# Kernel optimization log

Measured on AMD Instinct MI355X. Metric: run time of the kernel, lower is better.

Reference implementation:

```python
import jax, jax.numpy as jnp
from jax import lax
import numpy as np

B, CIN, HC, K, REC = 64, 64, 64, 3, 5
MG = 240 // REC  # 48
EPS = 1e-8


def conv2d(x, w, b, pad):
    y = lax.conv_general_dilated(x, w, (1, 1), [(pad, pad), (pad, pad)],
                                 dimension_numbers=('NCHW', 'OIHW', 'NCHW'))
    return y + b[None, :, None, None]


def conv_transpose2d(x, w, b, stride, pad):
    # PyTorch ConvTranspose2d: w is (Cin, Cout, kH, kW)
    k = w.shape[2]
    w_t = jnp.transpose(w[:, :, ::-1, ::-1], (1, 0, 2, 3))  # -> OIHW, flipped
    y = lax.conv_general_dilated(x, w_t, (1, 1),
                                 [(k - 1 - pad, k - 1 - pad)] * 2,
                                 lhs_dilation=(stride, stride),
                                 dimension_numbers=('NCHW', 'OIHW', 'NCHW'))
    return y + b[None, :, None, None]


def leaky(x):
    return jnp.where(x >= 0, x, 0.2 * x)


def setup_inputs() -> dict:
    key = jax.random.key(0)
    ks = jax.random.split(key, 12)
    s = 0.05
    return {
        'x': jax.random.normal(ks[0], (B, CIN, 64, 64), jnp.float32),
        'h': jax.random.normal(ks[1], (B, HC, 64, 64), jnp.float32),
        'c': jax.random.normal(ks[2], (B, HC, 64, 64), jnp.float32),
        'recalled_memory_feature': jax.random.normal(ks[3], (B, REC, MG, 32, 32), jnp.float32),
        'conv_w': jax.random.normal(ks[4], (5 * HC, CIN + HC, K, K), jnp.float32) * s,
        'conv_b': jax.random.normal(ks[5], (5 * HC,), jnp.float32) * s,
        'convc_w': jax.random.normal(ks[6], (MG, HC, 1, 1), jnp.float32) * s,
        'convc_b': jax.random.normal(ks[7], (MG,), jnp.float32) * s,
        'convssm_w': jax.random.normal(ks[8], (MG, MG, 4, 4), jnp.float32) * s,
        'convssm_b': jax.random.normal(ks[9], (MG,), jnp.float32) * s,
        'convfuse_w': jax.random.normal(ks[10], (HC, MG + HC, 1, 1), jnp.float32) * s,
        'convfuse_b': jax.random.normal(ks[11], (HC,), jnp.float32) * s,
    }


def reference(x, h, c, recalled_memory_feature, conv_w, conv_b, convc_w, convc_b,
              convssm_w, convssm_b, convfuse_w, convfuse_b):
    rm = recalled_memory_feature.reshape(B, REC, MG, 32, 32)
    rm_avg = rm.mean(axis=(3, 4))                      # (B, REC, MG)
    q = leaky(conv2d(c, convc_w, convc_b, 0))          # (B, MG, 64, 64)
    q_avg = q.mean(axis=(2, 3))                        # (B, MG)
    # cosine similarity along channel dim, vectorized over (B, REC)
    qn = jnp.maximum(jnp.linalg.norm(q_avg, axis=1, keepdims=True), EPS)   # (B,1)
    mn = jnp.maximum(jnp.linalg.norm(rm_avg, axis=2), EPS)                  # (B,REC)
    cos = jnp.einsum('bm,brm->br', q_avg, rm_avg) / (qn * mn)               # (B,REC)
    attn = jax.nn.softmax(cos, axis=1)                                      # (B,REC)
    mt = jnp.einsum('br,brmhw->bmhw', attn, rm)        # (B, MG, 32, 32)
    mt = leaky(conv_transpose2d(mt, convssm_w, convssm_b, 2, 1))  # (B, MG, 64, 64)

    gates = conv2d(jnp.concatenate((x, h), axis=1), conv_w, conv_b, K // 2)
    i, f, g, o, lam = jnp.split(gates, 5, axis=1)
    i = jax.nn.sigmoid(i)
    f = jax.nn.sigmoid(f)
    o = jax.nn.sigmoid(o)
    g = jnp.tanh(g)
    lam = jax.nn.sigmoid(lam)
    c_new = f * c + i * g
    h_new = o * jnp.tanh(conv2d(jnp.concatenate((c_new, mt), axis=1), convfuse_w, convfuse_b, 0))
    h_out = lam * h_new + (1.0 - lam) * h
    return (h_out, c_new)
```

## Files before the change

kernel.cpp:

```cpp
#include <hip/hip_runtime.h>
#include <hip/hip_bf16.h>
#include <cstdint>

#define HW 4096
#define MGc 48
#define RECc 5

typedef __attribute__((ext_vector_type(8))) short bf16x8;
typedef __attribute__((ext_vector_type(4))) float f32x4;

__device__ __forceinline__ float sigf(float x) { return 1.f / (1.f + expf(-x)); }
__device__ __forceinline__ float leakyf(float x) { return x >= 0.f ? x : 0.2f * x; }
__device__ __forceinline__ unsigned short f2bfu(float f) {
  __hip_bfloat16 b = __float2bfloat16(f);
  return *reinterpret_cast<unsigned short*>(&b);
}
__device__ __forceinline__ float bfu2f(unsigned short u) {
  unsigned v = ((unsigned)u) << 16;
  return __uint_as_float(v);
}
__device__ __forceinline__ void gload_lds16(const void* g, void* l) {
  __builtin_amdgcn_global_load_lds(
      (const __attribute__((address_space(1))) unsigned int*)g,
      (__attribute__((address_space(3))) unsigned int*)l, 16, 0, 0);
}

__global__ __launch_bounds__(256) void k_att(const float* __restrict__ rm,
    float* __restrict__ rm_sum, const float* __restrict__ c,
    const float* __restrict__ ccw, const float* __restrict__ ccb,
    float* __restrict__ q_part) {
  __shared__ __align__(16) char smem[13568];
  int bid = blockIdx.x, tid = threadIdx.x;
  if (bid < 15360) {
    float* sred = (float*)smem;
    int row = bid;
    const float4* p = reinterpret_cast<const float4*>(rm + (size_t)row * 1024);
    float4 v = p[tid];
    float s = v.x + v.y + v.z + v.w;
    #pragma unroll
    for (int off = 32; off; off >>= 1) s += __shfl_down(s, off);
    if ((tid & 63) == 0) sred[tid >> 6] = s;
    __syncthreads();
    if (tid == 0) rm_sum[row] = sred[0] + sred[1] + sred[2] + sred[3];
  } else {
    float* wl = (float*)smem;
    float* bl = wl + MGc * 64;
    float (*red)[MGc] = (float(*)[MGc])(bl + 64);
    int r = bid - 15360;
    int seg = r & 15, b = r >> 4;
    for (int i = tid; i < MGc * 64; i += 256) wl[i] = ccw[i];
    if (tid < MGc) bl[tid] = ccb[tid];
    __syncthreads();
    int px = seg * 256 + tid;
    float acc[MGc];
    #pragma unroll
    for (int m = 0; m < MGc; m++) acc[m] = 0.f;
    const float* cp = c + (size_t)b * 64 * HW + px;
    for (int ci = 0; ci < 64; ci++) {
      float v = cp[(size_t)ci * HW];
      #pragma unroll
      for (int m = 0; m < MGc; m++) acc[m] += wl[m * 64 + ci] * v;
    }
    int lane = tid & 63, wv = tid >> 6;
    #pragma unroll
    for (int m = 0; m < MGc; m++) {
      float t2 = leakyf(acc[m] + bl[m]);
      #pragma unroll
      for (int off = 32; off; off >>= 1) t2 += __shfl_down(t2, off);
      if (lane == 0) red[wv][m] = t2;
    }
    __syncthreads();
    if (tid < MGc) {
      float t2 = red[0][tid] + red[1][tid] + red[2][tid] + red[3][tid];
      q_part[((size_t)b * 16 + seg) * MGc + tid] = t2;
    }
  }
}

__global__ __launch_bounds__(256) void k_mid(const float* __restrict__ rm,
    const float* __restrict__ rm_sum, const float* __restrict__ q_part,
    float* __restrict__ mt_pre, const float* __restrict__ cw,
    __hip_bfloat16* __restrict__ Wp, __hip_bfloat16* __restrict__ Pp,
    const float* __restrict__ xin, const float* __restrict__ hin) {
  __shared__ __align__(16) char smem[16704];
  int bid = blockIdx.x, tid = threadIdx.x;
  if (bid < 12288) {
    float* sat = (float*)smem;
    int idx = bid * 256 + tid;
    int b = idx / (MGc * 1024);
    if (tid < 64) {
      int lane = tid;
      float q = 0.f;
      if (lane < MGc) {
        float s = 0.f;
        for (int sg = 0; sg < 16; sg++) s += q_part[((size_t)b * 16 + sg) * MGc + lane];
        q = s * (1.f / 4096.f);
      }
      float qs = q * q;
      #pragma unroll
      for (int off = 32; off; off >>= 1) qs += __shfl_xor(qs, off);
      float qn = fmaxf(sqrtf(qs), 1e-8f);
      float cosv[RECc];
      #pragma unroll
      for (int r = 0; r < RECc; r++) {
        float m = 0.f;
        if (lane < MGc) m = rm_sum[((size_t)b * RECc + r) * MGc + lane] * (1.f / 1024.f);
        float d = q * m, ms = m * m;
        #pragma unroll
        for (int off = 32; off; off >>= 1) { d += __shfl_xor(d, off); ms += __shfl_xor(ms, off); }
        float mn = fmaxf(sqrtf(ms), 1e-8f);
        cosv[r] = d / (qn * mn);
      }
      float mx = cosv[0];
      #pragma unroll
      for (int r = 1; r < RECc; r++) mx = fmaxf(mx, cosv[r]);
      float ssum = 0.f;
      #pragma unroll
      for (int r = 0; r < RECc; r++) { cosv[r] = expf(cosv[r] - mx); ssum += cosv[r]; }
      float inv = 1.f / ssum;
      #pragma unroll
      for (int r = 0; r < RECc; r++)
        if (lane == r) sat[r] = cosv[r] * inv;
    }
    __syncthreads();
    int rem = idx - b * (MGc * 1024);
    const float* base = rm + (size_t)b * RECc * MGc * 1024 + rem;
    float v = sat[0] * base[0] + sat[1] * base[MGc * 1024] + sat[2] * base[2 * MGc * 1024]
            + sat[3] * base[3 * MGc * 1024] + sat[4] * base[4 * MGc * 1024];
    mt_pre[idx] = v;
  } else if (bid < 13728) {
    int idx = (bid - 12288) * 256 + tid;
    int t = idx / (320 * 128);
    int rem = idx % (320 * 128);
    int ocp = rem / 128, ci = rem % 128;
    int nt = ocp / 80, r2 = ocp % 80, gate = r2 / 16, ml = r2 % 16;
    int oc = gate * 64 + nt * 16 + ml;
    Wp[idx] = __float2bfloat16(cw[((size_t)oc * 128 + ci) * 9 + t]);
  } else if (bid < 14768) {
    int idx = (bid - 13728) * 256 + tid;
    int b = idx / 4160, i = idx % 4160;
    bf16x8* base = reinterpret_cast<bf16x8*>(Pp);
    size_t u;
    if (i < 2112) {
      int r = (i < 1056) ? 0 : 65;
      int j = (i < 1056) ? i : i - 1056;
      u = ((size_t)b * 66 + r) * 1056 + j;
    } else {
      int i2 = i - 2112;
      int row = 1 + (i2 >> 5), k = i2 & 31;
      int px = (k < 16) ? 0 : 65, ci8 = k & 15;
      u = (((size_t)b * 66 + row) * 66 + px) * 16 + ci8;
    }
    base[u] = (bf16x8)0;
  } else {
    float (*t)[65] = (float(*)[65])smem;
    int r = bid - 14768;
    int half = r & 1, y = (r >> 1) & 63, b = r >> 7;
    const float* src = (half ? hin : xin) + (size_t)b * 64 * HW + y * 64;
    #pragma unroll
    for (int it = 0; it < 4; it++) {
      int li = it * 256 + tid;
      int ci = li >> 4, x4 = (li & 15) * 4;
      float4 v = *reinterpret_cast<const float4*>(src + (size_t)ci * HW + x4);
      t[x4][ci] = v.x; t[x4 + 1][ci] = v.y; t[x4 + 2][ci] = v.z; t[x4 + 3][ci] = v.w;
    }
    __syncthreads();
    int x = tid >> 2, c16 = (tid & 3) * 16;
    unsigned short* dst = reinterpret_cast<unsigned short*>(Pp) +
        ((((size_t)b * 66 + y + 1) * 66 + x + 1) * 128 + half * 64 + c16);
    bf16x8 o0, o1;
    #pragma unroll
    for (int j = 0; j < 8; j++) {
      o0[j] = (short)f2bfu(t[x][c16 + j]);
      o1[j] = (short)f2bfu(t[x][c16 + 8 + j]);
    }
    *reinterpret_cast<bf16x8*>(dst) = o0;
    *reinterpret_cast<bf16x8*>(dst + 8) = o1;
  }
}

__global__ __launch_bounds__(512) void k_ssm(const float* __restrict__ mt_pre,
    const float* __restrict__ w, const float* __restrict__ bias,
    __hip_bfloat16* __restrict__ mt) {
  __shared__ float in_t[12][10][20];
  __shared__ float w_t[12][48][16];
  int b = blockIdx.y;
  int tile = blockIdx.x;
  int y0 = (tile >> 1) * 16, x0 = (tile & 1) * 32;
  int wv = threadIdx.x >> 6, lane = threadIdx.x & 63;
  int co0 = wv * 6;
  int oyl = lane >> 2, xseg = lane & 3;
  int oy = y0 + oyl;
  int iy0 = (y0 >> 1) - 1, ix0 = (x0 >> 1) - 1;
  int kyA = (oy + 1) & 1;
  int iyA = (oy + 1 - kyA) >> 1;
  int rA = iyA - iy0, rB = rA - 1;
  float acc[6][8] = {};
  for (int ch = 0; ch < 4; ch++) {
    int ci0 = ch * 12;
    __syncthreads();
    for (int i = threadIdx.x; i < 12 * 10 * 18; i += 512) {
      int ci = i / 180, rr = (i % 180) / 18, cc2 = i % 18;
      int giy = iy0 + rr, gix = ix0 + cc2;
      float v = 0.f;
      if ((unsigned)giy < 32u && (unsigned)gix < 32u)
        v = mt_pre[(((size_t)b * MGc + ci0 + ci) * 32 + giy) * 32 + gix];
      in_t[ci][rr][cc2] = v;
    }
    for (int i = threadIdx.x; i < 12 * 48 * 16; i += 512)
      (&w_t[0][0][0])[i] = w[ci0 * 768 + i];
    __syncthreads();
    #pragma unroll 1
    for (int ci = 0; ci < 12; ci++) {
      float4 a0 = *reinterpret_cast<const float4*>(&in_t[ci][rA][xseg * 4]);
      float4 a1 = *reinterpret_cast<const float4*>(&in_t[ci][rA][xseg * 4 + 4]);
      float4 b0 = *reinterpret_cast<const float4*>(&in_t[ci][rB][xseg * 4]);
      float4 b1 = *reinterpret_cast<const float4*>(&in_t[ci][rB][xseg * 4 + 4]);
      float vA[6] = {a0.x, a0.y, a0.z, a0.w, a1.x, a1.y};
      float vB[6] = {b0.x, b0.y, b0.z, b0.w, b1.x, b1.y};
      #pragma unroll
      for (int co = 0; co < 6; co++) {
        const float* wp = &w_t[ci][co0 + co][0];
        float4 wA = *reinterpret_cast<const float4*>(wp + kyA * 4);
        float4 wB = *reinterpret_cast<const float4*>(wp + (kyA + 2) * 4);
        #pragma unroll
        for (int j = 0; j < 8; j++) {
          if ((j & 1) == 0) {
            int hi = (j >> 1) + 1, lo = j >> 1;
            acc[co][j] += vA[hi] * wA.y + vA[lo] * wA.w + vB[hi] * wB.y + vB[lo] * wB.w;
          } else {
            int hi = ((j + 1) >> 1) + 1, lo = (j + 1) >> 1;
            acc[co][j] += vA[hi] * wA.x + vA[lo] * wA.z + vB[hi] * wB.x + vB[lo] * wB.z;
          }
        }
      }
    }
  }
  int oxb = x0 + xseg * 8;
  #pragma unroll
  for (int co = 0; co < 6; co++) {
    float bb = bias[co0 + co];
    size_t obase = (((size_t)b * MGc + co0 + co) * 64 + oy) * 64 + oxb;
    #pragma unroll
    for (int j = 0; j < 8; j++)
      mt[obase + j] = __float2bfloat16(leakyf(acc[co][j] + bb));
  }
}

__global__ __launch_bounds__(256) void k_gates_mfma(
    const __hip_bfloat16* __restrict__ Pp, const __hip_bfloat16* __restrict__ Wp,
    const float* __restrict__ c, const float* __restrict__ cb,
    float* __restrict__ c_new, __hip_bfloat16* __restrict__ o_g,
    __hip_bfloat16* __restrict__ lam_g) {
  __shared__ bf16x8 s_in[1296];
  __shared__ bf16x8 s_w[2880];
  int orig = blockIdx.y * gridDim.x + blockIdx.x;
  int t_id = (orig & 7) * 512 + (orig >> 3);
  int b = t_id >> 6;
  int r6 = t_id & 63;
  int ytile = r6 >> 4, xtile = (r6 >> 2) & 3, nt = r6 & 3;
  int y0 = ytile * 16, x0 = xtile * 16;
  int tid = threadIdx.x;
  int wv = tid >> 6, lane = tid & 63;
  int lane15 = lane & 15, lq = lane >> 4;

  const char* Pb = (const char*)Pp;
  const char* Wb = (const char*)Wp;

  const char* gin[6]; int din[6]; bool ain[6];
  #pragma unroll
  for (int k = 0; k < 6; k++) {
    int u = wv + 4 * k;
    int e = u * 64 + lane;
    ain[k] = (u < 21) && (e < 1296);
    int ee = (e < 1296) ? e : 0;
    int L = ee / 72, r = ee - L * 72;
    int llq = r / 18, xi = r - llq * 18;
    gin[k] = Pb + ((((size_t)b * 66 + y0 + L) * 66 + (x0 + xi)) * 256) + llq * 16;
    din[k] = ee;
  }
  const char* gw[12]; int dw[12]; bool aw[12];
  #pragma unroll
  for (int k = 0; k < 12; k++) {
    int u = wv + 4 * k;
    aw[k] = (u < 45);
    int uu = (u < 45) ? u : 0;
    int e = uu * 64 + lane;
    int unit = e / 80, ol = e - unit * 80;
    int t = unit >> 2, g = unit & 3;
    gw[k] = Wb + (((size_t)t * 320 + nt * 80 + ol) * 128 + g * 8) * 2;
    dw[k] = e;
  }

  f32x4 acc[4][5];
  #pragma unroll
  for (int i = 0; i < 4; i++)
    #pragma unroll
    for (int j = 0; j < 5; j++) acc[i][j] = (f32x4)0.f;

  #pragma unroll 1
  for (int cc = 0; cc < 4; cc++) {
    __syncthreads();
    int co = cc * 64;
    #pragma unroll
    for (int k = 0; k < 6; k++)
      if (ain[k]) gload_lds16(gin[k] + co, (void*)&s_in[din[k]]);
    #pragma unroll
    for (int k = 0; k < 12; k++)
      if (aw[k]) gload_lds16(gw[k] + co, (void*)&s_w[dw[k]]);
    __syncthreads();

    #pragma unroll
    for (int dx = 0; dx < 3; dx++) {
      bf16x8 af[6];
      #pragma unroll
      for (int r = 0; r < 6; r++)
        af[r] = s_in[((wv * 4 + r) * 4 + lq) * 18 + lane15 + dx];
      #pragma unroll
      for (int ky = 0; ky < 3; ky++) {
        int t = ky * 3 + dx;
        bf16x8 bw[5];
        #pragma unroll
        for (int gg = 0; gg < 5; gg++)
          bw[gg] = s_w[(t * 4 + lq) * 80 + gg * 16 + lane15];
        __builtin_amdgcn_s_setprio(1);
        #pragma unroll
        for (int rr = 0; rr < 4; rr++)
          #pragma unroll
          for (int gg = 0; gg < 5; gg++)
            acc[rr][gg] = __builtin_amdgcn_mfma_f32_16x16x32_bf16(
                af[rr + ky], bw[gg], acc[rr][gg], 0, 0, 0);
        __builtin_amdgcn_s_setprio(0);
      }
    }
  }

  int m_hid = nt * 16 + lane15;
  float bi = cb[m_hid], bff = cb[64 + m_hid], bgg = cb[128 + m_hid],
        bo = cb[192 + m_hid], bl = cb[256 + m_hid];
  int xb = x0 + lq * 4;
  size_t chofs = ((size_t)b * 64 + m_hid) * HW;
  #pragma unroll
  for (int rr = 0; rr < 4; rr++) {
    int y = y0 + wv * 4 + rr;
    size_t pofs = chofs + (size_t)y * 64 + xb;
    f32x4 cold = *reinterpret_cast<const f32x4*>(c + pofs);
    f32x4 cn;
    unsigned short ov[4], lv[4];
    #pragma unroll
    for (int e = 0; e < 4; e++) {
      float i_ = sigf(acc[rr][0][e] + bi);
      float f_ = sigf(acc[rr][1][e] + bff);
      float g_ = tanhf(acc[rr][2][e] + bgg);
      float o_ = sigf(acc[rr][3][e] + bo);
      float l_ = sigf(acc[rr][4][e] + bl);
      cn[e] = f_ * cold[e] + i_ * g_;
      ov[e] = f2bfu(o_);
      lv[e] = f2bfu(l_);
    }
    *reinterpret_cast<f32x4*>(c_new + pofs) = cn;
    ushort4 ovv = {ov[0], ov[1], ov[2], ov[3]};
    ushort4 lvv = {lv[0], lv[1], lv[2], lv[3]};
    *reinterpret_cast<ushort4*>(reinterpret_cast<unsigned short*>(o_g) + pofs) = ovv;
    *reinterpret_cast<ushort4*>(reinterpret_cast<unsigned short*>(lam_g) + pofs) = lvv;
  }
}

__global__ __launch_bounds__(256) void k_fuse(const float* __restrict__ c_new,
    const __hip_bfloat16* __restrict__ mt, const __hip_bfloat16* __restrict__ o_g,
    const __hip_bfloat16* __restrict__ lam_g, const float* __restrict__ h,
    const float* __restrict__ fw, const float* __restrict__ fb,
    float* __restrict__ h_out) {
  __shared__ float wl[112][32];
  int b = blockIdx.y;
  int seg = blockIdx.x & 7, chalf = blockIdx.x >> 3;
  int co0 = chalf * 32;
  for (int i = threadIdx.x; i < 112 * 32; i += 256) {
    int ci = i >> 5, co = i & 31;
    wl[ci][co] = fw[(co0 + co) * 112 + ci];
  }
  __syncthreads();
  int px = seg * 512 + threadIdx.x * 2;
  size_t bofs = (size_t)b * 64 * HW;
  float2 acc[32];
  #pragma unroll
  for (int co = 0; co < 32; co++) { float bv = fb[co0 + co]; acc[co].x = bv; acc[co].y = bv; }
  #pragma unroll 1
  for (int ci = 0; ci < 64; ci++) {
    float2 v = *reinterpret_cast<const float2*>(c_new + bofs + (size_t)ci * HW + px);
    #pragma unroll
    for (int c4 = 0; c4 < 8; c4++) {
      float4 w = *reinterpret_cast<const float4*>(&wl[ci][c4 * 4]);
      acc[c4 * 4 + 0].x += w.x * v.x; acc[c4 * 4 + 0].y += w.x * v.y;
      acc[c4 * 4 + 1].x += w.y * v.x; acc[c4 * 4 + 1].y += w.y * v.y;
      acc[c4 * 4 + 2].x += w.z * v.x; acc[c4 * 4 + 2].y += w.z * v.y;
      acc[c4 * 4 + 3].x += w.w * v.x; acc[c4 * 4 + 3].y += w.w * v.y;
    }
  }
  const unsigned short* mtu = reinterpret_cast<const unsigned short*>(mt);
  size_t mtofs = (size_t)b * MGc * HW + px;
  #pragma unroll 1
  for (int ci = 0; ci < 48; ci++) {
    unsigned u = *reinterpret_cast<const unsigned*>(mtu + mtofs + (size_t)ci * HW);
    float vx = bfu2f((unsigned short)(u & 0xffff));
    float vy = bfu2f((unsigned short)(u >> 16));
    #pragma unroll
    for (int c4 = 0; c4 < 8; c4++) {
      float4 w = *reinterpret_cast<const float4*>(&wl[64 + ci][c4 * 4]);
      acc[c4 * 4 + 0].x += w.x * vx; acc[c4 * 4 + 0].y += w.x * vy;
      acc[c4 * 4 + 1].x += w.y * vx; acc[c4 * 4 + 1].y += w.y * vy;
      acc[c4 * 4 + 2].x += w.z * vx; acc[c4 * 4 + 2].y += w.z * vy;
      acc[c4 * 4 + 3].x += w.w * vx; acc[c4 * 4 + 3].y += w.w * vy;
    }
  }
  const unsigned short* ou = reinterpret_cast<const unsigned short*>(o_g);
  const unsigned short* lu = reinterpret_cast<const unsigned short*>(lam_g);
  #pragma unroll
  for (int co = 0; co < 32; co++) {
    size_t ofs = bofs + (size_t)(co0 + co) * HW + px;
    unsigned uo = *reinterpret_cast<const unsigned*>(ou + ofs);
    unsigned ul = *reinterpret_cast<const unsigned*>(lu + ofs);
    float2 hv = *reinterpret_cast<const float2*>(h + ofs);
    float hnx = tanhf(acc[co].x), hny = tanhf(acc[co].y);
    float ox = bfu2f((unsigned short)(uo & 0xffff)), oy = bfu2f((unsigned short)(uo >> 16));
    float lx = bfu2f((unsigned short)(ul & 0xffff)), ly = bfu2f((unsigned short)(ul >> 16));
    float2 r;
    r.x = lx * (ox * hnx) + (1.f - lx) * hv.x;
    r.y = ly * (oy * hny) + (1.f - ly) * hv.y;
    *reinterpret_cast<float2*>(h_out + ofs) = r;
  }
}

extern "C" void kernel_launch(void* const* d_in, const int* in_sizes, int n_in,
                              void* d_out, int out_size, void* d_ws, size_t ws_size,
                              hipStream_t stream) {
  const float* x   = (const float*)d_in[0];
  const float* h   = (const float*)d_in[1];
  const float* c   = (const float*)d_in[2];
  const float* rm  = (const float*)d_in[3];
  const float* cw  = (const float*)d_in[4];
  const float* cb  = (const float*)d_in[5];
  const float* ccw = (const float*)d_in[6];
  const float* ccb = (const float*)d_in[7];
  const float* sw  = (const float*)d_in[8];
  const float* sb  = (const float*)d_in[9];
  const float* fw  = (const float*)d_in[10];
  const float* fb  = (const float*)d_in[11];

  float* h_out = (float*)d_out;
  float* c_new = h_out + (size_t)16777216;

  char* ws = (char*)d_ws;
  float* rm_sum = (float*)(ws + 0);
  float* q_part = (float*)(ws + 65536);
  __hip_bfloat16* o_g   = (__hip_bfloat16*)(ws + 0);
  __hip_bfloat16* lam_g = (__hip_bfloat16*)(ws + 33554432);
  __hip_bfloat16* mt    = (__hip_bfloat16*)(ws + 67108864);
  __hip_bfloat16* Pp    = (__hip_bfloat16*)(ws + 92274688);
  __hip_bfloat16* Wp    = (__hip_bfloat16*)(ws + 163643392);
  float* mt_pre = h_out;

  k_att<<<16384, 256, 0, stream>>>(rm, rm_sum, c, ccw, ccb, q_part);
  k_mid<<<22960, 256, 0, stream>>>(rm, rm_sum, q_part, mt_pre, cw, Wp, Pp, x, h);
  k_ssm<<<dim3(8, 64), 512, 0, stream>>>(mt_pre, sw, sb, mt);
  k_gates_mfma<<<dim3(64, 64), 256, 0, stream>>>(Pp, Wp, c, cb, c_new, o_g, lam_g);
  k_fuse<<<dim3(16, 64), 256, 0, stream>>>(c_new, mt, o_g, lam_g, h, fw, fb, h_out);
}
```

Measured before the change: 637.4 us.

## Merge SSM transposed-conv into gates MFMA launch and widen fuse per-thread work

```diff
diff --git a/kernel.cpp b/kernel.cpp
--- a/kernel.cpp
+++ b/kernel.cpp
@@ -23,6 +23,9 @@
   __builtin_amdgcn_global_load_lds(
       (const __attribute__((address_space(1))) unsigned int*)g,
       (__attribute__((address_space(3))) unsigned int*)l, 16, 0, 0);
+}
+__device__ __forceinline__ void fma4(f32x4& a, float w, const f32x4& v) {
+  a[0] += w * v[0]; a[1] += w * v[1]; a[2] += w * v[2]; a[3] += w * v[3];
 }
 
 __global__ __launch_bounds__(256) void k_att(const float* __restrict__ rm,
@@ -179,190 +182,190 @@
   }
 }
 
-__global__ __launch_bounds__(512) void k_ssm(const float* __restrict__ mt_pre,
-    const float* __restrict__ w, const float* __restrict__ bias,
-    __hip_bfloat16* __restrict__ mt) {
-  __shared__ float in_t[12][10][20];
-  __shared__ float w_t[12][48][16];
-  int b = blockIdx.y;
-  int tile = blockIdx.x;
-  int y0 = (tile >> 1) * 16, x0 = (tile & 1) * 32;
-  int wv = threadIdx.x >> 6, lane = threadIdx.x & 63;
-  int co0 = wv * 6;
-  int oyl = lane >> 2, xseg = lane & 3;
-  int oy = y0 + oyl;
-  int iy0 = (y0 >> 1) - 1, ix0 = (x0 >> 1) - 1;
-  int kyA = (oy + 1) & 1;
-  int iyA = (oy + 1 - kyA) >> 1;
-  int rA = iyA - iy0, rB = rA - 1;
-  float acc[6][8] = {};
-  for (int ch = 0; ch < 4; ch++) {
-    int ci0 = ch * 12;
-    __syncthreads();
-    for (int i = threadIdx.x; i < 12 * 10 * 18; i += 512) {
-      int ci = i / 180, rr = (i % 180) / 18, cc2 = i % 18;
-      int giy = iy0 + rr, gix = ix0 + cc2;
-      float v = 0.f;
-      if ((unsigned)giy < 32u && (unsigned)gix < 32u)
-        v = mt_pre[(((size_t)b * MGc + ci0 + ci) * 32 + giy) * 32 + gix];
-      in_t[ci][rr][cc2] = v;
-    }
-    for (int i = threadIdx.x; i < 12 * 48 * 16; i += 512)
-      (&w_t[0][0][0])[i] = w[ci0 * 768 + i];
-    __syncthreads();
-    #pragma unroll 1
-    for (int ci = 0; ci < 12; ci++) {
-      float4 a0 = *reinterpret_cast<const float4*>(&in_t[ci][rA][xseg * 4]);
-      float4 a1 = *reinterpret_cast<const float4*>(&in_t[ci][rA][xseg * 4 + 4]);
-      float4 b0 = *reinterpret_cast<const float4*>(&in_t[ci][rB][xseg * 4]);
-      float4 b1 = *reinterpret_cast<const float4*>(&in_t[ci][rB][xseg * 4 + 4]);
-      float vA[6] = {a0.x, a0.y, a0.z, a0.w, a1.x, a1.y};
-      float vB[6] = {b0.x, b0.y, b0.z, b0.w, b1.x, b1.y};
-      #pragma unroll
-      for (int co = 0; co < 6; co++) {
-        const float* wp = &w_t[ci][co0 + co][0];
-        float4 wA = *reinterpret_cast<const float4*>(wp + kyA * 4);
-        float4 wB = *reinterpret_cast<const float4*>(wp + (kyA + 2) * 4);
-        #pragma unroll
-        for (int j = 0; j < 8; j++) {
-          if ((j & 1) == 0) {
-            int hi = (j >> 1) + 1, lo = j >> 1;
-            acc[co][j] += vA[hi] * wA.y + vA[lo] * wA.w + vB[hi] * wB.y + vB[lo] * wB.w;
-          } else {
-            int hi = ((j + 1) >> 1) + 1, lo = (j + 1) >> 1;
-            acc[co][j] += vA[hi] * wA.x + vA[lo] * wA.z + vB[hi] * wB.x + vB[lo] * wB.z;
-          }
-        }
-      }
-    }
-  }
-  int oxb = x0 + xseg * 8;
-  #pragma unroll
-  for (int co = 0; co < 6; co++) {
-    float bb = bias[co0 + co];
-    size_t obase = (((size_t)b * MGc + co0 + co) * 64 + oy) * 64 + oxb;
-    #pragma unroll
-    for (int j = 0; j < 8; j++)
-      mt[obase + j] = __float2bfloat16(leakyf(acc[co][j] + bb));
-  }
-}
-
-__global__ __launch_bounds__(256) void k_gates_mfma(
+__global__ __launch_bounds__(256) void k_main(
     const __hip_bfloat16* __restrict__ Pp, const __hip_bfloat16* __restrict__ Wp,
     const float* __restrict__ c, const float* __restrict__ cb,
     float* __restrict__ c_new, __hip_bfloat16* __restrict__ o_g,
-    __hip_bfloat16* __restrict__ lam_g) {
-  __shared__ bf16x8 s_in[1296];
-  __shared__ bf16x8 s_w[2880];
-  int orig = blockIdx.y * gridDim.x + blockIdx.x;
-  int t_id = (orig & 7) * 512 + (orig >> 3);
-  int b = t_id >> 6;
-  int r6 = t_id & 63;
-  int ytile = r6 >> 4, xtile = (r6 >> 2) & 3, nt = r6 & 3;
-  int y0 = ytile * 16, x0 = xtile * 16;
-  int tid = threadIdx.x;
-  int wv = tid >> 6, lane = tid & 63;
-  int lane15 = lane & 15, lq = lane >> 4;
-
-  const char* Pb = (const char*)Pp;
-  const char* Wb = (const char*)Wp;
-
-  const char* gin[6]; int din[6]; bool ain[6];
-  #pragma unroll
-  for (int k = 0; k < 6; k++) {
-    int u = wv + 4 * k;
-    int e = u * 64 + lane;
-    ain[k] = (u < 21) && (e < 1296);
-    int ee = (e < 1296) ? e : 0;
-    int L = ee / 72, r = ee - L * 72;
-    int llq = r / 18, xi = r - llq * 18;
-    gin[k] = Pb + ((((size_t)b * 66 + y0 + L) * 66 + (x0 + xi)) * 256) + llq * 16;
-    din[k] = ee;
-  }
-  const char* gw[12]; int dw[12]; bool aw[12];
-  #pragma unroll
-  for (int k = 0; k < 12; k++) {
-    int u = wv + 4 * k;
-    aw[k] = (u < 45);
-    int uu = (u < 45) ? u : 0;
-    int e = uu * 64 + lane;
-    int unit = e / 80, ol = e - unit * 80;
-    int t = unit >> 2, g = unit & 3;
-    gw[k] = Wb + (((size_t)t * 320 + nt * 80 + ol) * 128 + g * 8) * 2;
-    dw[k] = e;
-  }
-
-  f32x4 acc[4][5];
-  #pragma unroll
-  for (int i = 0; i < 4; i++)
-    #pragma unroll
-    for (int j = 0; j < 5; j++) acc[i][j] = (f32x4)0.f;
-
-  #pragma unroll 1
-  for (int cc = 0; cc < 4; cc++) {
-    __syncthreads();
-    int co = cc * 64;
-    #pragma unroll
-    for (int k = 0; k < 6; k++)
-      if (ain[k]) gload_lds16(gin[k] + co, (void*)&s_in[din[k]]);
-    #pragma unroll
-    for (int k = 0; k < 12; k++)
-      if (aw[k]) gload_lds16(gw[k] + co, (void*)&s_w[dw[k]]);
-    __syncthreads();
-
-    #pragma unroll
-    for (int dx = 0; dx < 3; dx++) {
-      bf16x8 af[6];
-      #pragma unroll
-      for (int r = 0; r < 6; r++)
-        af[r] = s_in[((wv * 4 + r) * 4 + lq) * 18 + lane15 + dx];
-      #pragma unroll
-      for (int ky = 0; ky < 3; ky++) {
-        int t = ky * 3 + dx;
-        bf16x8 bw[5];
+    __hip_bfloat16* __restrict__ lam_g,
+    const float* __restrict__ mt_pre, const float* __restrict__ sw,
+    const float* __restrict__ sb, __hip_bfloat16* __restrict__ mt) {
+  __shared__ __align__(16) char arena[66816];
+  int bid = blockIdx.x, tid = threadIdx.x;
+  if (bid < 4096) {
+    bf16x8* s_in = (bf16x8*)arena;
+    bf16x8* s_w  = (bf16x8*)(arena + 20736);
+    int t_id = (bid & 7) * 512 + (bid >> 3);
+    int b = t_id >> 6;
+    int r6 = t_id & 63;
+    int ytile = r6 >> 4, xtile = (r6 >> 2) & 3, nt = r6 & 3;
+    int y0 = ytile * 16, x0 = xtile * 16;
+    int wv = tid >> 6, lane = tid & 63;
+    int lane15 = lane & 15, lq = lane >> 4;
+
+    const char* Pb = (const char*)Pp;
+    const char* Wb = (const char*)Wp;
+
+    const char* gin[6]; int din[6]; bool ain[6];
+    #pragma unroll
+    for (int k = 0; k < 6; k++) {
+      int u = wv + 4 * k;
+      int e = u * 64 + lane;
+      ain[k] = (u < 21) && (e < 1296);
+      int ee = (e < 1296) ? e : 0;
+      int L = ee / 72, r = ee - L * 72;
+      int llq = r / 18, xi = r - llq * 18;
+      gin[k] = Pb + ((((size_t)b * 66 + y0 + L) * 66 + (x0 + xi)) * 256) + llq * 16;
+      din[k] = ee;
+    }
+    const char* gw[12]; int dw[12]; bool aw[12];
+    #pragma unroll
+    for (int k = 0; k < 12; k++) {
+      int u = wv + 4 * k;
+      aw[k] = (u < 45);
+      int uu = (u < 45) ? u : 0;
+      int e = uu * 64 + lane;
+      int unit = e / 80, ol = e - unit * 80;
+      int t = unit >> 2, g = unit & 3;
+      gw[k] = Wb + (((size_t)t * 320 + nt * 80 + ol) * 128 + g * 8) * 2;
+      dw[k] = e;
+    }
+
+    f32x4 acc[4][5];
+    #pragma unroll
+    for (int i = 0; i < 4; i++)
+      #pragma unroll
+      for (int j = 0; j < 5; j++) acc[i][j] = (f32x4)0.f;
+
+    #pragma unroll 1
+    for (int cc = 0; cc < 4; cc++) {
+      __syncthreads();
+      int co = cc * 64;
+      #pragma unroll
+      for (int k = 0; k < 6; k++)
+        if (ain[k]) gload_lds16(gin[k] + co, (void*)&s_in[din[k]]);
+      #pragma unroll
+      for (int k = 0; k < 12; k++)
+        if (aw[k]) gload_lds16(gw[k] + co, (void*)&s_w[dw[k]]);
+      __syncthreads();
+
+      #pragma unroll
+      for (int dx = 0; dx < 3; dx++) {
+        bf16x8 af[6];
         #pragma unroll
-        for (int gg = 0; gg < 5; gg++)
-          bw[gg] = s_w[(t * 4 + lq) * 80 + gg * 16 + lane15];
-        __builtin_amdgcn_s_setprio(1);
+        for (int r = 0; r < 6; r++)
+          af[r] = s_in[((wv * 4 + r) * 4 + lq) * 18 + lane15 + dx];
         #pragma unroll
-        for (int rr = 0; rr < 4; rr++)
+        for (int ky = 0; ky < 3; ky++) {
+          int t = ky * 3 + dx;
+          bf16x8 bw[5];
           #pragma unroll
           for (int gg = 0; gg < 5; gg++)
-            acc[rr][gg] = __builtin_amdgcn_mfma_f32_16x16x32_bf16(
-                af[rr + ky], bw[gg], acc[rr][gg], 0, 0, 0);
-        __builtin_amdgcn_s_setprio(0);
-      }
-    }
-  }
-
-  int m_hid = nt * 16 + lane15;
-  float bi = cb[m_hid], bff = cb[64 + m_hid], bgg = cb[128 + m_hid],
-        bo = cb[192 + m_hid], bl = cb[256 + m_hid];
-  int xb = x0 + lq * 4;
-  size_t chofs = ((size_t)b * 64 + m_hid) * HW;
-  #pragma unroll
-  for (int rr = 0; rr < 4; rr++) {
-    int y = y0 + wv * 4 + rr;
-    size_t pofs = chofs + (size_t)y * 64 + xb;
-    f32x4 cold = *reinterpret_cast<const f32x4*>(c + pofs);
-    f32x4 cn;
-    unsigned short ov[4], lv[4];
-    #pragma unroll
-    for (int e = 0; e < 4; e++) {
-      float i_ = sigf(acc[rr][0][e] + bi);
-      float f_ = sigf(acc[rr][1][e] + bff);
-      float g_ = tanhf(acc[rr][2][e] + bgg);
-      float o_ = sigf(acc[rr][3][e] + bo);
-      float l_ = sigf(acc[rr][4][e] + bl);
-      cn[e] = f_ * cold[e] + i_ * g_;
-      ov[e] = f2bfu(o_);
-      lv[e] = f2bfu(l_);
-    }
-    *reinterpret_cast<f32x4*>(c_new + pofs) = cn;
-    ushort4 ovv = {ov[0], ov[1], ov[2], ov[3]};
-    ushort4 lvv = {lv[0], lv[1], lv[2], lv[3]};
-    *reinterpret_cast<ushort4*>(reinterpret_cast<unsigned short*>(o_g) + pofs) = ovv;
-    *reinterpret_cast<ushort4*>(reinterpret_cast<unsigned short*>(lam_g) + pofs) = lvv;
+            bw[gg] = s_w[(t * 4 + lq) * 80 + gg * 16 + lane15];
+          __builtin_amdgcn_s_setprio(1);
+          #pragma unroll
+          for (int rr = 0; rr < 4; rr++)
+            #pragma unroll
+            for (int gg = 0; gg < 5; gg++)
+              acc[rr][gg] = __builtin_amdgcn_mfma_f32_16x16x32_bf16(
+                  af[rr + ky], bw[gg], acc[rr][gg], 0, 0, 0);
+          __builtin_amdgcn_s_setprio(0);
+        }
+      }
+    }
+
+    int m_hid = nt * 16 + lane15;
+    float bi = cb[m_hid], bff = cb[64 + m_hid], bgg = cb[128 + m_hid],
+          bo = cb[192 + m_hid], bl = cb[256 + m_hid];
+    int xb = x0 + lq * 4;
+    size_t chofs = ((size_t)b * 64 + m_hid) * HW;
+    #pragma unroll
+    for (int rr = 0; rr < 4; rr++) {
+      int y = y0 + wv * 4 + rr;
+      size_t pofs = chofs + (size_t)y * 64 + xb;
+      f32x4 cold = *reinterpret_cast<const f32x4*>(c + pofs);
+      f32x4 cn;
+      unsigned short ov[4], lv[4];
+      #pragma unroll
+      for (int e = 0; e < 4; e++) {
+        float i_ = sigf(acc[rr][0][e] + bi);
+        float f_ = sigf(acc[rr][1][e] + bff);
+        float g_ = tanhf(acc[rr][2][e] + bgg);
+        float o_ = sigf(acc[rr][3][e] + bo);
+        float l_ = sigf(acc[rr][4][e] + bl);
+        cn[e] = f_ * cold[e] + i_ * g_;
+        ov[e] = f2bfu(o_);
+        lv[e] = f2bfu(l_);
+      }
+      *reinterpret_cast<f32x4*>(c_new + pofs) = cn;
+      ushort4 ovv = {ov[0], ov[1], ov[2], ov[3]};
+      ushort4 lvv = {lv[0], lv[1], lv[2], lv[3]};
+      *reinterpret_cast<ushort4*>(reinterpret_cast<unsigned short*>(o_g) + pofs) = ovv;
+      *reinterpret_cast<ushort4*>(reinterpret_cast<unsigned short*>(lam_g) + pofs) = lvv;
+    }
+  } else {
+    float (*in_t)[10][20] = (float(*)[10][20])arena;
+    float (*w_t)[48][16]  = (float(*)[48][16])(arena + 9600);
+    int sbid = bid - 4096;
+    int tile = sbid & 7, b = sbid >> 3;
+    int y0 = (tile >> 1) * 16, x0 = (tile & 1) * 32;
+    int wv = tid >> 6, lane = tid & 63;
+    int co0 = wv * 12;
+    int oyl = lane >> 2, xseg = lane & 3;
+    int oy = y0 + oyl;
+    int iy0 = (y0 >> 1) - 1, ix0 = (x0 >> 1) - 1;
+    int kyA = (oy + 1) & 1;
+    int iyA = (oy + 1 - kyA) >> 1;
+    int rA = iyA - iy0, rB = rA - 1;
+    float acc[12][8] = {};
+    for (int ch = 0; ch < 4; ch++) {
+      int ci0 = ch * 12;
+      __syncthreads();
+      for (int i = tid; i < 12 * 10 * 18; i += 256) {
+        int ci = i / 180, rr = (i % 180) / 18, cc2 = i % 18;
+        int giy = iy0 + rr, gix = ix0 + cc2;
+        float v = 0.f;
+        if ((unsigned)giy < 32u && (unsigned)gix < 32u)
+          v = mt_pre[(((size_t)b * MGc + ci0 + ci) * 32 + giy) * 32 + gix];
+        in_t[ci][rr][cc2] = v;
+      }
+      for (int i = tid; i < 12 * 48 * 16; i += 256)
+        (&w_t[0][0][0])[i] = sw[ci0 * 768 + i];
+      __syncthreads();
+      #pragma unroll 1
+      for (int ci = 0; ci < 12; ci++) {
+        float4 a0 = *reinterpret_cast<const float4*>(&in_t[ci][rA][xseg * 4]);
+        float4 a1 = *reinterpret_cast<const float4*>(&in_t[ci][rA][xseg * 4 + 4]);
+        float4 b0 = *reinterpret_cast<const float4*>(&in_t[ci][rB][xseg * 4]);
+        float4 b1 = *reinterpret_cast<const float4*>(&in_t[ci][rB][xseg * 4 + 4]);
+        float vA[6] = {a0.x, a0.y, a0.z, a0.w, a1.x, a1.y};
+        float vB[6] = {b0.x, b0.y, b0.z, b0.w, b1.x, b1.y};
+        #pragma unroll
+        for (int co = 0; co < 12; co++) {
+          const float* wp = &w_t[ci][co0 + co][0];
+          float4 wA = *reinterpret_cast<const float4*>(wp + kyA * 4);
+          float4 wB = *reinterpret_cast<const float4*>(wp + (kyA + 2) * 4);
+          #pragma unroll
+          for (int j = 0; j < 8; j++) {
+            if ((j & 1) == 0) {
+              int hi = (j >> 1) + 1, lo = j >> 1;
+              acc[co][j] += vA[hi] * wA.y + vA[lo] * wA.w + vB[hi] * wB.y + vB[lo] * wB.w;
+            } else {
+              int hi = ((j + 1) >> 1) + 1, lo = (j + 1) >> 1;
+              acc[co][j] += vA[hi] * wA.x + vA[lo] * wA.z + vB[hi] * wB.x + vB[lo] * wB.z;
+            }
+          }
+        }
+      }
+    }
+    int oxb = x0 + xseg * 8;
+    #pragma unroll
+    for (int co = 0; co < 12; co++) {
+      float bb = sb[co0 + co];
+      size_t obase = (((size_t)b * MGc + co0 + co) * 64 + oy) * 64 + oxb;
+      #pragma unroll
+      for (int j = 0; j < 8; j++)
+        mt[obase + j] = __float2bfloat16(leakyf(acc[co][j] + bb));
+    }
   }
 }
 
@@ -373,44 +376,44 @@
     float* __restrict__ h_out) {
   __shared__ float wl[112][32];
   int b = blockIdx.y;
-  int seg = blockIdx.x & 7, chalf = blockIdx.x >> 3;
+  int seg = blockIdx.x & 3, chalf = blockIdx.x >> 2;
   int co0 = chalf * 32;
   for (int i = threadIdx.x; i < 112 * 32; i += 256) {
     int ci = i >> 5, co = i & 31;
     wl[ci][co] = fw[(co0 + co) * 112 + ci];
   }
   __syncthreads();
-  int px = seg * 512 + threadIdx.x * 2;
+  int px = seg * 1024 + threadIdx.x * 4;
   size_t bofs = (size_t)b * 64 * HW;
-  float2 acc[32];
+  f32x4 acc[32];
   #pragma unroll
-  for (int co = 0; co < 32; co++) { float bv = fb[co0 + co]; acc[co].x = bv; acc[co].y = bv; }
+  for (int co = 0; co < 32; co++) acc[co] = (f32x4)(fb[co0 + co]);
   #pragma unroll 1
   for (int ci = 0; ci < 64; ci++) {
-    float2 v = *reinterpret_cast<const float2*>(c_new + bofs + (size_t)ci * HW + px);
+    f32x4 v = *reinterpret_cast<const f32x4*>(c_new + bofs + (size_t)ci * HW + px);
     #pragma unroll
     for (int c4 = 0; c4 < 8; c4++) {
       float4 w = *reinterpret_cast<const float4*>(&wl[ci][c4 * 4]);
-      acc[c4 * 4 + 0].x += w.x * v.x; acc[c4 * 4 + 0].y += w.x * v.y;
-      acc[c4 * 4 + 1].x += w.y * v.x; acc[c4 * 4 + 1].y += w.y * v.y;
-      acc[c4 * 4 + 2].x += w.z * v.x; acc[c4 * 4 + 2].y += w.z * v.y;
-      acc[c4 * 4 + 3].x += w.w * v.x; acc[c4 * 4 + 3].y += w.w * v.y;
+      fma4(acc[c4 * 4 + 0], w.x, v);
+      fma4(acc[c4 * 4 + 1], w.y, v);
+      fma4(acc[c4 * 4 + 2], w.z, v);
+      fma4(acc[c4 * 4 + 3], w.w, v);
     }
   }
   const unsigned short* mtu = reinterpret_cast<const unsigned short*>(mt);
   size_t mtofs = (size_t)b * MGc * HW + px;
   #pragma unroll 1
   for (int ci = 0; ci < 48; ci++) {
-    unsigned u = *reinterpret_cast<const unsigned*>(mtu + mtofs + (size_t)ci * HW);
-    float vx = bfu2f((unsigned short)(u & 0xffff));
-    float vy = bfu2f((unsigned short)(u >> 16));
+    ushort4 u = *reinterpret_cast<const ushort4*>(mtu + mtofs + (size_t)ci * HW);
+    f32x4 v;
+    v[0] = bfu2f(u.x); v[1] = bfu2f(u.y); v[2] = bfu2f(u.z); v[3] = bfu2f(u.w);
     #pragma unroll
     for (int c4 = 0; c4 < 8; c4++) {
       float4 w = *reinterpret_cast<const float4*>(&wl[64 + ci][c4 * 4]);
-      acc[c4 * 4 + 0].x += w.x * vx; acc[c4 * 4 + 0].y += w.x * vy;
-      acc[c4 * 4 + 1].x += w.y * vx; acc[c4 * 4 + 1].y += w.y * vy;
-      acc[c4 * 4 + 2].x += w.z * vx; acc[c4 * 4 + 2].y += w.z * vy;
-      acc[c4 * 4 + 3].x += w.w * vx; acc[c4 * 4 + 3].y += w.w * vy;
+      fma4(acc[c4 * 4 + 0], w.x, v);
+      fma4(acc[c4 * 4 + 1], w.y, v);
+      fma4(acc[c4 * 4 + 2], w.z, v);
+      fma4(acc[c4 * 4 + 3], w.w, v);
     }
   }
   const unsigned short* ou = reinterpret_cast<const unsigned short*>(o_g);
@@ -418,16 +421,20 @@
   #pragma unroll
   for (int co = 0; co < 32; co++) {
     size_t ofs = bofs + (size_t)(co0 + co) * HW + px;
-    unsigned uo = *reinterpret_cast<const unsigned*>(ou + ofs);
-    unsigned ul = *reinterpret_cast<const unsigned*>(lu + ofs);
-    float2 hv = *reinterpret_cast<const float2*>(h + ofs);
-    float hnx = tanhf(acc[co].x), hny = tanhf(acc[co].y);
-    float ox = bfu2f((unsigned short)(uo & 0xffff)), oy = bfu2f((unsigned short)(uo >> 16));
-    float lx = bfu2f((unsigned short)(ul & 0xffff)), ly = bfu2f((unsigned short)(ul >> 16));
-    float2 r;
-    r.x = lx * (ox * hnx) + (1.f - lx) * hv.x;
-    r.y = ly * (oy * hny) + (1.f - ly) * hv.y;
-    *reinterpret_cast<float2*>(h_out + ofs) = r;
+    ushort4 uo = *reinterpret_cast<const ushort4*>(ou + ofs);
+    ushort4 ul = *reinterpret_cast<const ushort4*>(lu + ofs);
+    f32x4 hv = *reinterpret_cast<const f32x4*>(h + ofs);
+    const unsigned short* uop = &uo.x;
+    const unsigned short* ulp = &ul.x;
+    f32x4 r;
+    #pragma unroll
+    for (int e = 0; e < 4; e++) {
+      float hn = tanhf(acc[co][e]);
+      float o = bfu2f(uop[e]);
+      float l = bfu2f(ulp[e]);
+      r[e] = l * (o * hn) + (1.f - l) * hv[e];
+    }
+    *reinterpret_cast<f32x4*>(h_out + ofs) = r;
   }
 }
 
@@ -462,7 +469,6 @@
 
   k_att<<<16384, 256, 0, stream>>>(rm, rm_sum, c, ccw, ccb, q_part);
   k_mid<<<22960, 256, 0, stream>>>(rm, rm_sum, q_part, mt_pre, cw, Wp, Pp, x, h);
-  k_ssm<<<dim3(8, 64), 512, 0, stream>>>(mt_pre, sw, sb, mt);
-  k_gates_mfma<<<dim3(64, 64), 256, 0, stream>>>(Pp, Wp, c, cb, c_new, o_g, lam_g);
-  k_fuse<<<dim3(16, 64), 256, 0, stream>>>(c_new, mt, o_g, lam_g, h, fw, fb, h_out);
-}
+  k_main<<<4608, 256, 0, stream>>>(Pp, Wp, c, cb, c_new, o_g, lam_g, mt_pre, sw, sb, mt);
+  k_fuse<<<dim3(8, 64), 256, 0, stream>>>(c_new, mt, o_g, lam_g, h, fw, fb, h_out);
+}
```

New measurement: 635.7 us. About the same (-0.3%).
